# Kernel tuning notes

Hardware: AMD Instinct MI355X
Metric: run time of the kernel (lower is better)

## Reference

```python
import jax, jax.numpy as jnp
import numpy as np

B, S, F, H = 16, 2048, 1024, 16
D = F // H
EPS = 1e-5


def setup_inputs() -> dict:
    key = jax.random.key(0)
    ks = jax.random.split(key, 10)
    scale = 1.0 / np.sqrt(F)
    return {
        "x": jax.random.normal(ks[0], (B, S, F), jnp.float32),
        "Wq": jax.random.normal(ks[1], (F, F), jnp.float32) * scale,
        "bq": jnp.zeros((F,), jnp.float32),
        "Wk": jax.random.normal(ks[2], (F, F), jnp.float32) * scale,
        "bk": jnp.zeros((F,), jnp.float32),
        "Wv": jax.random.normal(ks[3], (F, F), jnp.float32) * scale,
        "bv": jnp.zeros((F,), jnp.float32),
        "Wo": jax.random.normal(ks[4], (F, F), jnp.float32) * scale,
        "bo": jnp.zeros((F,), jnp.float32),
        "gamma": jnp.ones((F,), jnp.float32),
        "beta": jnp.zeros((F,), jnp.float32),
    }


def reference(x, Wq, bq, Wk, bk, Wv, bv, Wo, bo, gamma, beta):
    # x: (B, S, F). Dropout is identity in eval mode.
    b, s, f = x.shape
    q = (x @ Wq + bq).reshape(b, s, H, D)
    k = (x @ Wk + bk).reshape(b, s, H, D)
    v = (x @ Wv + bv).reshape(b, s, H, D)
    # Faithful to source: the einsum (applied to permuted tensors) contracts
    # across HEADS at each sequence position -> scores (B, S, H, H).
    energy = jnp.einsum('bshd,bsgd->bshg', q, k) / (D ** 0.5)
    attn = jax.nn.softmax(energy, axis=-1)  # softmax over key-head axis
    out = jnp.einsum('bshg,bsgd->bshd', attn, v).reshape(b, s, f)
    out = out @ Wo + bo
    # LayerNorm over last dim (eps=1e-5, affine)
    mu = jnp.mean(out, axis=-1, keepdims=True)
    var = jnp.mean((out - mu) ** 2, axis=-1, keepdims=True)
    return (out - mu) * jax.lax.rsqrt(var + EPS) * gamma + beta
```

## Files before the change

### kernel.cpp

```cpp
#include <hip/hip_runtime.h>
#include <hip/hip_bf16.h>
#include <stdint.h>

#define MM   32768
#define FFD  1024
#define NQKV 3072

typedef __bf16 bf16x8 __attribute__((ext_vector_type(8)));
typedef float  f32x4  __attribute__((ext_vector_type(4)));

__device__ __forceinline__ unsigned short f2bf_bits(float f){
  __hip_bfloat16 h = __float2bfloat16(f);
  unsigned short u;
  __builtin_memcpy(&u, &h, 2);
  return u;
}

__device__ __forceinline__ float bf2f(unsigned short u){
  unsigned v = ((unsigned)u) << 16;
  float f;
  __builtin_memcpy(&f, &v, 4);
  return f;
}

__device__ __forceinline__ void gld16(const void* g, void* l){
  const unsigned int* gu = (const unsigned int*)g;
  unsigned int* lu = (unsigned int*)l;
  __builtin_amdgcn_global_load_lds(
      (const __attribute__((address_space(1))) unsigned int*)gu,
      (__attribute__((address_space(3))) unsigned int*)lu,
      16, 0, 0);
}

#define BARRIER() do { asm volatile("" ::: "memory"); \
                       __builtin_amdgcn_s_barrier();  \
                       asm volatile("" ::: "memory"); } while(0)

__global__ __launch_bounds__(256) void k_convert_bf16(const float* __restrict__ in,
                                                      unsigned short* __restrict__ out,
                                                      int n4){
  int i = blockIdx.x * 256 + threadIdx.x;
  if (i >= n4) return;
  float4 v = ((const float4*)in)[i];
  ushort4 r;
  r.x = f2bf_bits(v.x); r.y = f2bf_bits(v.y);
  r.z = f2bf_bits(v.z); r.w = f2bf_bits(v.w);
  ((ushort4*)out)[i] = r;
}

__global__ __launch_bounds__(256) void k_transpose4(const float* __restrict__ Wq,
                                                    const float* __restrict__ Wk,
                                                    const float* __restrict__ Wv,
                                                    const float* __restrict__ Wo,
                                                    unsigned short* __restrict__ Wqkv_t,
                                                    unsigned short* __restrict__ Wo_t){
  __shared__ float tile[32][33];
  const float* in;
  unsigned short* out;
  switch (blockIdx.z){
    case 0:  in = Wq; out = Wqkv_t;               break;
    case 1:  in = Wk; out = Wqkv_t + 1024 * 1024; break;
    case 2:  in = Wv; out = Wqkv_t + 2048 * 1024; break;
    default: in = Wo; out = Wo_t;                 break;
  }
  int bc = blockIdx.x * 32, br = blockIdx.y * 32;
  int tx = threadIdx.x & 31, ty = threadIdx.x >> 5;
  #pragma unroll
  for (int j = 0; j < 32; j += 8)
    tile[ty + j][tx] = in[(size_t)(br + ty + j) * 1024 + bc + tx];
  __syncthreads();
  #pragma unroll
  for (int j = 0; j < 32; j += 8)
    out[(size_t)(bc + ty + j) * 1024 + br + tx] = f2bf_bits(tile[tx][ty + j]);
}

__global__ __launch_bounds__(256, 2) void k_gemm_bt(
    const unsigned short* __restrict__ A,
    const unsigned short* __restrict__ Bt,
    const float* __restrict__ b0, const float* __restrict__ b1, const float* __restrict__ b2,
    unsigned short* __restrict__ Cout, int M, int N, int K)
{
  __shared__ alignas(16) char smem[73728];

  const int tid  = threadIdx.x;
  const int lane = tid & 63;
  const int wave = tid >> 6;
  const int wr = wave >> 1, wc = wave & 1;
  const int quad = lane >> 4, lrow = lane & 15;
  const int csw = ((quad ^ (lrow & 3)) << 4);

  const int nwgx = gridDim.x;
  int nwg = nwgx * gridDim.y;
  int bid = blockIdx.y * nwgx + blockIdx.x;
  int cpx = nwg >> 3;
  int nid = (bid & 7) * cpx + (bid >> 3);
  int by = nid / nwgx;
  int bx = nid - by * nwgx;

  const long rowBase = (long)by * 256;
  const long colBase = (long)bx * 128;

  f32x4 acc[8][4];
  #pragma unroll
  for (int i = 0; i < 8; i++)
    #pragma unroll
    for (int j = 0; j < 4; j++)
      acc[i][j] = (f32x4){0.f, 0.f, 0.f, 0.f};

  const int swz8 = 8 * ((tid & 3) ^ ((tid >> 2) & 3));
  const unsigned short* gA = A  + (rowBase + (tid >> 2)) * (long)K + swz8;
  const unsigned short* gB = Bt + (colBase + (tid >> 2)) * (long)K + swz8;
  const long r64 = 64L * K;
  const int t16 = tid * 16;

  const int nk = K >> 5;

  auto STAGE = [&](int u, int s){
    char* base = smem + s * 24576;
    const unsigned short* a = gA + (long)u * 32;
    const unsigned short* b = gB + (long)u * 32;
    gld16(a,           base +         t16);
    gld16(a + r64,     base +  4096 + t16);
    gld16(a + 2 * r64, base +  8192 + t16);
    gld16(a + 3 * r64, base + 12288 + t16);
    gld16(b,           base + 16384 + t16);
    gld16(b + r64,     base + 20480 + t16);
  };

  STAGE(0, 0);
  STAGE(1, 1);

  for (int t = 0; t < nk; ++t){
    if (t < nk - 1) asm volatile("s_waitcnt vmcnt(6)" ::: "memory");
    else            asm volatile("s_waitcnt vmcnt(0)" ::: "memory");
    BARRIER();

    char* buf = smem + (t % 3) * 24576;
    if (t < nk - 2) STAGE(t + 2, (t + 2) % 3);

    bf16x8 bfr[4];
    const char* bb = buf + 16384 + wc * 4096 + lrow * 64 + csw;
    #pragma unroll
    for (int n = 0; n < 4; ++n)
      bfr[n] = *(const bf16x8*)(bb + n * 1024);

    #pragma unroll
    for (int p = 0; p < 2; ++p){
      bf16x8 af[4];
      const char* ab = buf + wr * 8192 + p * 4096 + lrow * 64 + csw;
      #pragma unroll
      for (int f = 0; f < 4; ++f)
        af[f] = *(const bf16x8*)(ab + f * 1024);
      __builtin_amdgcn_s_setprio(1);
      #pragma unroll
      for (int f = 0; f < 4; ++f)
        #pragma unroll
        for (int n = 0; n < 4; ++n)
          acc[p * 4 + f][n] =
              __builtin_amdgcn_mfma_f32_16x16x32_bf16(af[f], bfr[n], acc[p * 4 + f][n], 0, 0, 0);
      __builtin_amdgcn_s_setprio(0);
    }
  }

  BARRIER();
  #pragma unroll
  for (int n = 0; n < 4; ++n){
    int lcol = wc * 64 + n * 16 + lrow;
    long col = colBase + lcol;
    const float* bp = (col < 1024) ? b0 : ((col < 2048) ? b1 : b2);
    float bias = bp[col & 1023];
    #pragma unroll
    for (int m = 0; m < 8; ++m){
      int row0 = wr * 128 + (m >> 2) * 64 + (m & 3) * 16 + quad * 4;
      #pragma unroll
      for (int r = 0; r < 4; ++r){
        float v = acc[m][n][r] + bias;
        int byte = (row0 + r) * 256 + ((lcol * 2) ^ (quad << 5));
        *(unsigned short*)(smem + byte) = f2bf_bits(v);
      }
    }
  }
  asm volatile("s_waitcnt lgkmcnt(0)" ::: "memory");
  BARRIER();
  #pragma unroll
  for (int i = 0; i < 16; ++i){
    int c = i * 256 + tid;
    int row = c >> 4, cidx = c & 15;
    int rb = (cidx ^ (((row >> 2) & 3) << 1)) * 16;
    uint4 u = *(const uint4*)(smem + row * 256 + rb);
    *(uint4*)(Cout + (rowBase + row) * (long)N + colBase + cidx * 8) = u;
  }
}

__global__ __launch_bounds__(256) void k_attention(const unsigned short* __restrict__ qkv,
                                                   unsigned short* __restrict__ aout){
  const int lane = threadIdx.x & 63;
  const int wave = threadIdx.x >> 6;
  const int pos  = blockIdx.x * 4 + wave;
  const int quad = lane >> 4, lidx = lane & 15;

  const unsigned short* src = qkv + (size_t)pos * 3072;

  f32x4 s = (f32x4){0.f, 0.f, 0.f, 0.f};
  #pragma unroll
  for (int kk = 0; kk < 2; ++kk){
    bf16x8 aK = *(const bf16x8*)(src + 1024 + lidx * 64 + kk * 32 + quad * 8);
    bf16x8 bQ = *(const bf16x8*)(src +        lidx * 64 + kk * 32 + quad * 8);
    s = __builtin_amdgcn_mfma_f32_16x16x32_bf16(aK, bQ, s, 0, 0, 0);
  }

  float v0 = s[0] * 0.125f, v1 = s[1] * 0.125f;
  float v2 = s[2] * 0.125f, v3 = s[3] * 0.125f;
  float m = fmaxf(fmaxf(v0, v1), fmaxf(v2, v3));
  m = fmaxf(m, __shfl_xor(m, 16));
  m = fmaxf(m, __shfl_xor(m, 32));
  float e0 = __expf(v0 - m), e1 = __expf(v1 - m);
  float e2 = __expf(v2 - m), e3 = __expf(v3 - m);
  float sum = e0 + e1 + e2 + e3;
  sum += __shfl_xor(sum, 16);
  sum += __shfl_xor(sum, 32);
  float inv = 1.0f / sum;
  unsigned P01 = (unsigned)f2bf_bits(e0 * inv) | ((unsigned)f2bf_bits(e1 * inv) << 16);
  unsigned P23 = (unsigned)f2bf_bits(e2 * inv) | ((unsigned)f2bf_bits(e3 * inv) << 16);

  int sA = ((quad * 32) + lidx) & 63;
  int sB = (sA + 16) & 63;
  unsigned w0 = (unsigned)__shfl((int)P01, sA);
  unsigned w1 = (unsigned)__shfl((int)P23, sA);
  unsigned w2 = (unsigned)__shfl((int)P01, sB);
  unsigned w3 = (unsigned)__shfl((int)P23, sB);
  if (quad >= 2){ w0 = 0u; w1 = 0u; w2 = 0u; w3 = 0u; }
  union { unsigned u[4]; bf16x8 v; } bp;
  bp.u[0] = w0; bp.u[1] = w1; bp.u[2] = w2; bp.u[3] = w3;

  const unsigned short* Vp = src + 2048;
  unsigned short* dst = aout + (size_t)pos * 1024;
  #pragma unroll
  for (int n4 = 0; n4 < 4; ++n4){
    union { unsigned short us[8]; bf16x8 v; } av;
    #pragma unroll
    for (int j = 0; j < 8; ++j){
      unsigned short rv = Vp[((quad * 8 + j) & 15) * 64 + n4 * 16 + lidx];
      av.us[j] = (quad < 2) ? rv : (unsigned short)0;
    }
    f32x4 o = __builtin_amdgcn_mfma_f32_16x16x32_bf16(
        av.v, bp.v, (f32x4){0.f, 0.f, 0.f, 0.f}, 0, 0, 0);
    unsigned lo = (unsigned)f2bf_bits(o[0]) | ((unsigned)f2bf_bits(o[1]) << 16);
    unsigned hi = (unsigned)f2bf_bits(o[2]) | ((unsigned)f2bf_bits(o[3]) << 16);
    uint2 st; st.x = lo; st.y = hi;
    *(uint2*)(dst + lidx * 64 + n4 * 16 + quad * 4) = st;
  }
}

__global__ __launch_bounds__(256) void k_ln_bf16(const unsigned short* __restrict__ ob,
                                                 const float* __restrict__ gamma,
                                                 const float* __restrict__ beta,
                                                 float* __restrict__ out){
  __shared__ float red[8];
  int tid = threadIdx.x;
  int row = blockIdx.x;
  ushort4 u = ((const ushort4*)(ob + (size_t)row * 1024))[tid];
  float x0 = bf2f(u.x), x1 = bf2f(u.y), x2 = bf2f(u.z), x3 = bf2f(u.w);
  float s  = x0 + x1 + x2 + x3;
  float ss = x0 * x0 + x1 * x1 + x2 * x2 + x3 * x3;
  #pragma unroll
  for (int off = 32; off > 0; off >>= 1){
    s  += __shfl_down(s, off);
    ss += __shfl_down(ss, off);
  }
  if ((tid & 63) == 0){ red[tid >> 6] = s; red[4 + (tid >> 6)] = ss; }
  __syncthreads();
  float S  = red[0] + red[1] + red[2] + red[3];
  float SS = red[4] + red[5] + red[6] + red[7];
  float mean = S * (1.0f / 1024.0f);
  float var  = SS * (1.0f / 1024.0f) - mean * mean;
  float rstd = rsqrtf(var + 1e-5f);
  float4 g = ((const float4*)gamma)[tid];
  float4 b = ((const float4*)beta)[tid];
  float4 v;
  v.x = (x0 - mean) * rstd * g.x + b.x;
  v.y = (x1 - mean) * rstd * g.y + b.y;
  v.z = (x2 - mean) * rstd * g.z + b.z;
  v.w = (x3 - mean) * rstd * g.w + b.w;
  ((float4*)(out + (size_t)row * 1024))[tid] = v;
}

extern "C" void kernel_launch(void* const* d_in, const int* in_sizes, int n_in,
                              void* d_out, int out_size, void* d_ws, size_t ws_size,
                              hipStream_t stream){
  const float* x     = (const float*)d_in[0];
  const float* Wq    = (const float*)d_in[1];
  const float* bq    = (const float*)d_in[2];
  const float* Wk    = (const float*)d_in[3];
  const float* bk    = (const float*)d_in[4];
  const float* Wv    = (const float*)d_in[5];
  const float* bv    = (const float*)d_in[6];
  const float* Wo    = (const float*)d_in[7];
  const float* bo    = (const float*)d_in[8];
  const float* gamma = (const float*)d_in[9];
  const float* beta  = (const float*)d_in[10];
  float* out = (float*)d_out;

  char* ws = (char*)d_ws;
  unsigned short* Wqkv_t = (unsigned short*)ws;
  unsigned short* Wo_t   = (unsigned short*)(ws + 6291456);
  unsigned short* xb     = (unsigned short*)(ws + 8388608);
  unsigned short* qkv    = (unsigned short*)(ws + 75497472);
  unsigned short* aout   = xb;
  unsigned short* obf    = qkv;

  k_convert_bf16<<<32768, 256, 0, stream>>>(x, xb, (MM * FFD) / 4);

  k_transpose4<<<dim3(32, 32, 4), 256, 0, stream>>>(Wq, Wk, Wv, Wo, Wqkv_t, Wo_t);

  k_gemm_bt<<<dim3(NQKV / 128, MM / 256), 256, 0, stream>>>(
      xb, Wqkv_t, bq, bk, bv, qkv, MM, NQKV, FFD);

  k_attention<<<MM / 4, 256, 0, stream>>>(qkv, aout);

  k_gemm_bt<<<dim3(FFD / 128, MM / 256), 256, 0, stream>>>(
      aout, Wo_t, bo, bo, bo, obf, MM, FFD, FFD);

  k_ln_bf16<<<MM, 256, 0, stream>>>(obf, gamma, beta, out);
}
```

Before: 626.6 us.

## Enlarge GEMM tile to 256x256 with 512 threads and four-stage LDS pipeline

The bf16 GEMM now uses a 256x256 output tile per workgroup with 8 waves instead of 256x128 with 4 waves. It also moves from a three-buffer to a four-buffer global-to-LDS prefetch ring with adjusted vmcnt waits, and updates the LDS swizzles and the epilogue staging layout to match. The aim is to halve B-operand traffic per output and hide more memory latency. In exchange each block uses 128KB of LDS, which likely limits occupancy to one block per CU, and the output projection launches far fewer workgroups, which risks poor load balance.

```diff
diff --git a/kernel.cpp b/kernel.cpp
--- a/kernel.cpp
+++ b/kernel.cpp
@@ -74,20 +74,20 @@
     out[(size_t)(bc + ty + j) * 1024 + br + tx] = f2bf_bits(tile[tx][ty + j]);
 }
 
-__global__ __launch_bounds__(256, 2) void k_gemm_bt(
+__global__ __launch_bounds__(512, 2) void k_gemm_bt(
     const unsigned short* __restrict__ A,
     const unsigned short* __restrict__ Bt,
     const float* __restrict__ b0, const float* __restrict__ b1, const float* __restrict__ b2,
     unsigned short* __restrict__ Cout, int M, int N, int K)
 {
-  __shared__ alignas(16) char smem[73728];
+  __shared__ alignas(16) char smem[131072];
 
   const int tid  = threadIdx.x;
   const int lane = tid & 63;
   const int wave = tid >> 6;
-  const int wr = wave >> 1, wc = wave & 1;
+  const int wr = wave >> 2, wc = wave & 3;
   const int quad = lane >> 4, lrow = lane & 15;
-  const int csw = ((quad ^ (lrow & 3)) << 4);
+  const int sa = ((lrow >> 1) & 3) << 4;
 
   const int nwgx = gridDim.x;
   int nwg = nwgx * gridDim.y;
@@ -98,7 +98,7 @@
   int bx = nid - by * nwgx;
 
   const long rowBase = (long)by * 256;
-  const long colBase = (long)bx * 128;
+  const long colBase = (long)bx * 256;
 
   f32x4 acc[8][4];
   #pragma unroll
@@ -107,39 +107,41 @@
     for (int j = 0; j < 4; j++)
       acc[i][j] = (f32x4){0.f, 0.f, 0.f, 0.f};
 
-  const int swz8 = 8 * ((tid & 3) ^ ((tid >> 2) & 3));
+  const int swz8 = 8 * ((tid & 3) ^ ((tid >> 3) & 3));
   const unsigned short* gA = A  + (rowBase + (tid >> 2)) * (long)K + swz8;
   const unsigned short* gB = Bt + (colBase + (tid >> 2)) * (long)K + swz8;
-  const long r64 = 64L * K;
-  const int t16 = tid * 16;
+  const long hstep = 128L * K;
 
   const int nk = K >> 5;
 
-  auto STAGE = [&](int u, int s){
-    char* base = smem + s * 24576;
-    const unsigned short* a = gA + (long)u * 32;
-    const unsigned short* b = gB + (long)u * 32;
-    gld16(a,           base +         t16);
-    gld16(a + r64,     base +  4096 + t16);
-    gld16(a + 2 * r64, base +  8192 + t16);
-    gld16(a + 3 * r64, base + 12288 + t16);
-    gld16(b,           base + 16384 + t16);
-    gld16(b + r64,     base + 20480 + t16);
-  };
-
-  STAGE(0, 0);
-  STAGE(1, 1);
+  #pragma unroll
+  for (int tt = 0; tt < 3; ++tt){
+    char* nb = smem + tt * 32768;
+    gld16(gA + tt * 32,         nb +         tid * 16);
+    gld16(gA + tt * 32 + hstep, nb +  8192 + tid * 16);
+    gld16(gB + tt * 32,         nb + 16384 + tid * 16);
+    gld16(gB + tt * 32 + hstep, nb + 24576 + tid * 16);
+  }
 
   for (int t = 0; t < nk; ++t){
-    if (t < nk - 1) asm volatile("s_waitcnt vmcnt(6)" ::: "memory");
-    else            asm volatile("s_waitcnt vmcnt(0)" ::: "memory");
+    if (t <= nk - 3)      asm volatile("s_waitcnt vmcnt(8)" ::: "memory");
+    else if (t == nk - 2) asm volatile("s_waitcnt vmcnt(4)" ::: "memory");
+    else                  asm volatile("s_waitcnt vmcnt(0)" ::: "memory");
     BARRIER();
 
-    char* buf = smem + (t % 3) * 24576;
-    if (t < nk - 2) STAGE(t + 2, (t + 2) % 3);
+    char* buf = smem + (t & 3) * 32768;
+    if (t < nk - 3){
+      char* nb = smem + ((t + 3) & 3) * 32768;
+      const unsigned short* sA = gA + (long)(t + 3) * 32;
+      const unsigned short* sB = gB + (long)(t + 3) * 32;
+      gld16(sA,         nb +         tid * 16);
+      gld16(sA + hstep, nb +  8192 + tid * 16);
+      gld16(sB,         nb + 16384 + tid * 16);
+      gld16(sB + hstep, nb + 24576 + tid * 16);
+    }
 
     bf16x8 bfr[4];
-    const char* bb = buf + 16384 + wc * 4096 + lrow * 64 + csw;
+    const char* bb = buf + 16384 + wc * 4096 + lrow * 64 + ((quad * 16) ^ sa);
     #pragma unroll
     for (int n = 0; n < 4; ++n)
       bfr[n] = *(const bf16x8*)(bb + n * 1024);
@@ -147,7 +149,7 @@
     #pragma unroll
     for (int p = 0; p < 2; ++p){
       bf16x8 af[4];
-      const char* ab = buf + wr * 8192 + p * 4096 + lrow * 64 + csw;
+      const char* ab = buf + wr * 8192 + p * 4096 + lrow * 64 + ((quad * 16) ^ sa);
       #pragma unroll
       for (int f = 0; f < 4; ++f)
         af[f] = *(const bf16x8*)(ab + f * 1024);
@@ -172,10 +174,11 @@
     #pragma unroll
     for (int m = 0; m < 8; ++m){
       int row0 = wr * 128 + (m >> 2) * 64 + (m & 3) * 16 + quad * 4;
+      int sw = ((row0 >> 2) & 3) << 5;
       #pragma unroll
       for (int r = 0; r < 4; ++r){
         float v = acc[m][n][r] + bias;
-        int byte = (row0 + r) * 256 + ((lcol * 2) ^ (quad << 5));
+        int byte = (row0 + r) * 512 + ((lcol * 2) ^ sw);
         *(unsigned short*)(smem + byte) = f2bf_bits(v);
       }
     }
@@ -184,10 +187,10 @@
   BARRIER();
   #pragma unroll
   for (int i = 0; i < 16; ++i){
-    int c = i * 256 + tid;
-    int row = c >> 4, cidx = c & 15;
+    int c = i * 512 + tid;
+    int row = c >> 5, cidx = c & 31;
     int rb = (cidx ^ (((row >> 2) & 3) << 1)) * 16;
-    uint4 u = *(const uint4*)(smem + row * 256 + rb);
+    uint4 u = *(const uint4*)(smem + row * 512 + rb);
     *(uint4*)(Cout + (rowBase + row) * (long)N + colBase + cidx * 8) = u;
   }
 }
@@ -313,12 +316,12 @@
 
   k_transpose4<<<dim3(32, 32, 4), 256, 0, stream>>>(Wq, Wk, Wv, Wo, Wqkv_t, Wo_t);
 
-  k_gemm_bt<<<dim3(NQKV / 128, MM / 256), 256, 0, stream>>>(
+  k_gemm_bt<<<dim3(NQKV / 256, MM / 256), 512, 0, stream>>>(
       xb, Wqkv_t, bq, bk, bv, qkv, MM, NQKV, FFD);
 
   k_attention<<<MM / 4, 256, 0, stream>>>(qkv, aout);
 
-  k_gemm_bt<<<dim3(FFD / 128, MM / 256), 256, 0, stream>>>(
+  k_gemm_bt<<<dim3(FFD / 256, MM / 256), 512, 0, stream>>>(
       aout, Wo_t, bo, bo, bo, obf, MM, FFD, FFD);
 
   k_ln_bf16<<<MM, 256, 0, stream>>>(obf, gamma, beta, out);
```

Result: faster. 611.3 us (-2.4%).
